# Kernel optimization log

Measured on AMD Instinct MI355X. Metric: run time of the kernel, lower is better.

Reference implementation:

```python
import jax, jax.numpy as jnp
import numpy as np

D = 768      # feature_dim (sum of extractor dims), divisible by nhead
H = 16       # nhead
DH = D // H
L = 3        # n_layers
NT = 256     # image tokens = (224/14)^2
B = 4
NPAST = 16
NF = 20      # hard-coded future horizon
C = NT + 1 + NPAST  # context length: image + intent + past
NEG = jnp.float32(-1e9)


def setup_inputs() -> dict:
    key = jax.random.key(0)
    ks = iter(jax.random.split(key, 64))
    def nrm(shape, scale):
        return jax.random.normal(next(ks), shape, jnp.float32) * scale
    w = lambda i, o: nrm((i, o), 1.0 / np.sqrt(i))
    inp = {}
    inp["image_tokens"] = nrm((B, NT, D), 1.0)
    inp["past"] = nrm((B, NPAST, 6), 1.0)
    inp["intent"] = jax.random.randint(next(ks), (B,), 1, 4)
    inp["pos_enc"] = nrm((1, NT, D), 0.02)          # positional_encoding param
    inp["future_q"] = nrm((1, NF, D), 1.0)           # future_queries param
    inp["intent_emb"] = nrm((1, 3, D), 1.0)          # intent_embeds param
    inp["time_emb"] = nrm((36, D), 1.0)              # time_embeds table
    inp["W_past"] = w(6, D);  inp["b_past"] = jnp.zeros((D,))
    inp["W_ppos"] = w(2, D);  inp["b_ppos"] = jnp.zeros((D,))
    inp["W_pp"] = w(2, D);    inp["b_pp"] = jnp.zeros((D,))      # pos_proj linear
    inp["g_pp"] = jnp.ones((D,)); inp["be_pp"] = jnp.zeros((D,)) # pos_proj LN
    inp["Wqkv"] = nrm((L, D, 3 * D), 1.0 / np.sqrt(D)); inp["bqkv"] = jnp.zeros((L, 3 * D))
    inp["Wo"] = nrm((L, D, D), 1.0 / np.sqrt(D));       inp["bo"] = jnp.zeros((L, D))
    inp["g1"] = jnp.ones((L, D)); inp["beta1"] = jnp.zeros((L, D))
    inp["g2"] = jnp.ones((L, D)); inp["beta2"] = jnp.zeros((L, D))
    inp["W1"] = nrm((L, D, 4 * D), 1.0 / np.sqrt(D));   inp["bf1"] = jnp.zeros((L, 4 * D))
    inp["W2"] = nrm((L, 4 * D, D), 1.0 / np.sqrt(4 * D)); inp["bf2"] = jnp.zeros((L, D))
    inp["Wd1"] = w(D, D); inp["bd1"] = jnp.zeros((D,))
    inp["Wd2"] = w(D, D); inp["bd2"] = jnp.zeros((D,))
    inp["Wd3"] = w(D, 2); inp["bd3"] = jnp.zeros((2,))
    return inp


def _ln(x, g, b):
    m = x.mean(-1, keepdims=True)
    v = ((x - m) ** 2).mean(-1, keepdims=True)
    return (x - m) / jnp.sqrt(v + 1e-5) * g + b


def reference(image_tokens, past, intent, pos_enc, future_q, intent_emb, time_emb,
              W_past, b_past, W_ppos, b_ppos, W_pp, b_pp, g_pp, be_pp,
              Wqkv, bqkv, Wo, bo, g1, beta1, g2, beta2, W1, bf1, W2, bf2,
              Wd1, bd1, Wd2, bd2, Wd3, bd3):
    Bn = past.shape[0]
    ctx_img = image_tokens + pos_enc                       # [B, NT, D]
    idx = jnp.clip(intent - 1, 0, 2)
    intent_tok = intent_emb[0][idx][:, None, :]            # [B, 1, D]
    past_tok = past @ W_past + b_past + past[..., :2] @ W_ppos + b_ppos + time_emb[:NPAST]
    context = jnp.concatenate([ctx_img, intent_tok, past_tok], axis=1)  # [B, C, D]
    future = jnp.broadcast_to(future_q + time_emb[NPAST:NPAST + NF], (Bn, NF, D))

    def block(x, mask, l):
        # norm_first TransformerEncoderLayer (dropout=0 at inference)
        h = _ln(x, g1[l], beta1[l])
        qkv = h @ Wqkv[l] + bqkv[l]
        q, k, v = jnp.split(qkv, 3, axis=-1)
        S = x.shape[1]
        q = q.reshape(Bn, S, H, DH).transpose(0, 2, 1, 3)
        k = k.reshape(Bn, S, H, DH).transpose(0, 2, 1, 3)
        v = v.reshape(Bn, S, H, DH).transpose(0, 2, 1, 3)
        scores = jnp.einsum('bhqd,bhkd->bhqk', q, k) / np.sqrt(DH).astype(np.float32) + mask
        a = jax.nn.softmax(scores, axis=-1)
        o = jnp.einsum('bhqk,bhkd->bhqd', a, v).transpose(0, 2, 1, 3).reshape(Bn, S, D)
        x = x + o @ Wo[l] + bo[l]
        h2 = _ln(x, g2[l], beta2[l])
        return x + jax.nn.relu(h2 @ W1[l] + bf1[l]) @ W2[l] + bf2[l]

    preds = []
    for t in range(NF):
        S = C + t + 1
        fm = jnp.where(jnp.triu(jnp.ones((t + 1, t + 1), bool), 1), NEG, jnp.float32(0.0))
        mask = jnp.zeros((S, S), jnp.float32).at[C:, C:].set(fm)
        x = jnp.concatenate([context, future[:, :t + 1]], axis=1)
        for l in range(L):
            x = block(x, mask, l)
        d = x[:, -1, :]
        d = jax.nn.gelu(d @ Wd1 + bd1, approximate=False)
        d = jax.nn.gelu(d @ Wd2 + bd2, approximate=False)
        p = d @ Wd3 + bd3                                   # [B, 2]
        preds.append(p[:, None, :])
        if t < NF - 1:
            future = future.at[:, t + 1].add(jax.nn.relu(_ln(p @ W_pp + b_pp, g_pp, be_pp)))
    return jnp.concatenate(preds, axis=1)                   # [B, 20, 2]
```

## Files before the change

kernel.cpp:

```cpp
#include <hip/hip_runtime.h>
#include <math.h>

#define DIM   768
#define NHEAD 16
#define DHEAD 48
#define NLAY  3
#define NTOK  256
#define BATCH 4
#define NPAST_ 16
#define NFUT  20
#define CCTX  273
#define SMAXT 293
#define MROWS 1172
#define NEGV  (-1.0e9f)
#define QKVPLANE 900096
#define STSTRIDE 52

typedef unsigned short u16;
typedef unsigned int   u32;
typedef __attribute__((ext_vector_type(8))) short short8;
typedef __attribute__((ext_vector_type(4))) float floatx4;

__device__ inline u16 f2bf(float x) {
    union { float f; u32 u; } v; v.f = x;
    u32 r = v.u + 0x7fffu + ((v.u >> 16) & 1u);
    return (u16)(r >> 16);
}

__device__ inline float bf2f(u16 x) {
    union { u32 u; float f; } c; c.u = ((u32)x) << 16;
    return c.f;
}

__device__ inline float gelu_f(float x) {
    return 0.5f * x * (1.0f + erff(x * 0.70710678118654752f));
}

__global__ void init_base(const float* __restrict__ img, const float* __restrict__ past,
                          const int* __restrict__ intent, const float* __restrict__ pos,
                          const float* __restrict__ futq, const float* __restrict__ iemb,
                          const float* __restrict__ temb, const float* __restrict__ Wp,
                          const float* __restrict__ bp, const float* __restrict__ Wpp,
                          const float* __restrict__ bpp, float* __restrict__ X)
{
    int r = blockIdx.x;
    int b = r / SMAXT, s = r % SMAXT;
    for (int j = threadIdx.x; j < DIM; j += blockDim.x) {
        float v;
        if (s < NTOK) {
            v = img[(long)(b * NTOK + s) * DIM + j] + pos[(long)s * DIM + j];
        } else if (s == NTOK) {
            int idx = intent[b] - 1; idx = idx < 0 ? 0 : (idx > 2 ? 2 : idx);
            v = iemb[(long)idx * DIM + j];
        } else if (s < CCTX) {
            int i = s - (NTOK + 1);
            v = bp[j] + bpp[j] + temb[(long)i * DIM + j];
            const float* pr = past + (long)(b * NPAST_ + i) * 6;
            #pragma unroll
            for (int c = 0; c < 6; ++c) v += pr[c] * Wp[(long)c * DIM + j];
            v += pr[0] * Wpp[j] + pr[1] * Wpp[DIM + j];
        } else {
            int f = s - CCTX;
            v = futq[(long)f * DIM + j] + temb[(long)(NPAST_ + f) * DIM + j];
        }
        X[(long)r * DIM + j] = v;
    }
}

__global__ void convert_transpose(const float* __restrict__ W, u16* __restrict__ Wt, int K, int N)
{
    __shared__ float tile[32][33];
    long lstride = (long)K * N;
    W  += blockIdx.z * lstride;
    Wt += blockIdx.z * lstride;
    int n0 = blockIdx.x * 32, k0 = blockIdx.y * 32;
    int tx = threadIdx.x & 31, ty = threadIdx.x >> 5;
    for (int i = ty; i < 32; i += 8)
        tile[i][tx] = W[(long)(k0 + i) * N + n0 + tx];
    __syncthreads();
    for (int i = ty; i < 32; i += 8)
        Wt[(long)(n0 + i) * K + k0 + tx] = f2bf(tile[tx][i]);
}

__launch_bounds__(256)
__global__ void ln_kernel(const float* __restrict__ x, const float* __restrict__ g,
                          const float* __restrict__ be, u16* __restrict__ y)
{
    int row = blockIdx.x * 4 + (threadIdx.x >> 6);
    int lane = threadIdx.x & 63;
    if (row >= MROWS) return;
    const float* xr = x + (long)row * DIM;
    float v[12];
    float s = 0.f;
    #pragma unroll
    for (int i = 0; i < 12; ++i) { v[i] = xr[lane + 64 * i]; s += v[i]; }
    for (int off = 32; off; off >>= 1) s += __shfl_down(s, off, 64);
    s = __shfl(s, 0, 64);
    float mean = s * (1.f / 768.f);
    float vs = 0.f;
    #pragma unroll
    for (int i = 0; i < 12; ++i) { float d = v[i] - mean; vs += d * d; }
    for (int off = 32; off; off >>= 1) vs += __shfl_down(vs, off, 64);
    vs = __shfl(vs, 0, 64);
    float inv = rsqrtf(vs * (1.f / 768.f) + 1e-5f);
    u16* yr = y + (long)row * DIM;
    #pragma unroll
    for (int i = 0; i < 12; ++i) {
        int j = lane + 64 * i;
        yr[j] = f2bf((v[i] - mean) * inv * g[j] + be[j]);
    }
}

__launch_bounds__(256)
__global__ void ln4_kernel(const float* __restrict__ x, const float* __restrict__ g,
                           const float* __restrict__ be, u16* __restrict__ y, int S)
{
    int b = threadIdx.x >> 6;
    int lane = threadIdx.x & 63;
    long row = (long)b * SMAXT + (S - 1);
    const float* xr = x + row * DIM;
    float v[12];
    float s = 0.f;
    #pragma unroll
    for (int i = 0; i < 12; ++i) { v[i] = xr[lane + 64 * i]; s += v[i]; }
    for (int off = 32; off; off >>= 1) s += __shfl_down(s, off, 64);
    s = __shfl(s, 0, 64);
    float mean = s * (1.f / 768.f);
    float vs = 0.f;
    #pragma unroll
    for (int i = 0; i < 12; ++i) { float d = v[i] - mean; vs += d * d; }
    for (int off = 32; off; off >>= 1) vs += __shfl_down(vs, off, 64);
    vs = __shfl(vs, 0, 64);
    float inv = rsqrtf(vs * (1.f / 768.f) + 1e-5f);
    u16* yr = y + row * DIM;
    #pragma unroll
    for (int i = 0; i < 12; ++i) {
        int j = lane + 64 * i;
        yr[j] = f2bf((v[i] - mean) * inv * g[j] + be[j]);
    }
}

template<int BM, int BN, int MODE>
__launch_bounds__(256)
__global__ void gemm_mfma(const u16* __restrict__ A, const u16* __restrict__ Wt,
                          const float* __restrict__ bias, const float* __restrict__ res,
                          void* __restrict__ outv, int M, int N, int K, int n0base)
{
    constexpr int MFRAG = BM / 16;
    constexpr int MI = MFRAG / 2;
    constexpr int NSUB = BN / 16;
    constexpr int NJ = NSUB / 2;
    constexpr int NA = (BM * 8) / 256;
    constexpr int NB = (BN * 8) / 256;
    __shared__ u16 As[2 * MFRAG * 64 * 8];
    __shared__ u16 Bs[2 * NSUB * 64 * 8];

    int tid = threadIdx.x;
    int lane = tid & 63;
    int w = tid >> 6, wm = w >> 1, wn = w & 1;
    int m0 = blockIdx.y * BM, n0 = n0base + blockIdx.x * BN;

    floatx4 acc[MI][NJ];
    #pragma unroll
    for (int i = 0; i < MI; ++i)
        #pragma unroll
        for (int j = 0; j < NJ; ++j) acc[i][j] = (floatx4){0.f, 0.f, 0.f, 0.f};

    int lm = lane & 15, lk = lane >> 4;

    for (int k0 = 0; k0 < K; k0 += 64) {
        __syncthreads();
        #pragma unroll
        for (int i = 0; i < NA; ++i) {
            int q = tid + 256 * i;
            int r = q >> 3, c = q & 7;
            int gr = m0 + r; if (gr >= M) gr = M - 1;
            int4 v = *(const int4*)(A + (long)gr * K + k0 + c * 8);
            int off = (((c >> 2) * MFRAG + (r >> 4)) * 64 + (r & 15) * 4 + (c & 3)) * 8;
            *(int4*)&As[off] = v;
        }
        #pragma unroll
        for (int i = 0; i < NB; ++i) {
            int q = tid + 256 * i;
            int r = q >> 3, c = q & 7;
            int4 v = *(const int4*)(Wt + (long)(n0 + r) * K + k0 + c * 8);
            int off = (((c >> 2) * NSUB + (r >> 4)) * 64 + (r & 15) * 4 + (c & 3)) * 8;
            *(int4*)&Bs[off] = v;
        }
        __syncthreads();
        #pragma unroll
        for (int t = 0; t < 2; ++t) {
            short8 af[MI];
            #pragma unroll
            for (int i = 0; i < MI; ++i)
                af[i] = *(const short8*)&As[((t * MFRAG + wm * MI + i) * 64 + lm * 4 + lk) * 8];
            short8 bfr[NJ];
            #pragma unroll
            for (int j = 0; j < NJ; ++j)
                bfr[j] = *(const short8*)&Bs[((t * NSUB + wn * NJ + j) * 64 + lm * 4 + lk) * 8];
            #pragma unroll
            for (int i = 0; i < MI; ++i)
                #pragma unroll
                for (int j = 0; j < NJ; ++j)
                    acc[i][j] = __builtin_amdgcn_mfma_f32_16x16x32_bf16(af[i], bfr[j], acc[i][j], 0, 0, 0);
        }
    }

    #pragma unroll
    for (int j = 0; j < NJ; ++j) {
        int col = n0 + wn * (NJ * 16) + j * 16 + lm;
        float bv = bias[col];
        #pragma unroll
        for (int i = 0; i < MI; ++i) {
            int rbase = m0 + wm * (MI * 16) + i * 16 + lk * 4;
            #pragma unroll
            for (int rr = 0; rr < 4; ++rr) {
                int row = rbase + rr;
                if (row >= M) continue;
                float val = acc[i][j][rr] + bv;
                if (MODE == 0) {
                    val += res[(long)row * N + col];
                    ((float*)outv)[(long)row * N + col] = val;
                } else if (MODE == 1) {
                    val = fmaxf(val, 0.f);
                    ((u16*)outv)[(long)row * N + col] = f2bf(val);
                } else {
                    int which = col >= 1536 ? 2 : (col >= 768 ? 1 : 0);
                    int rem = col - which * 768;
                    int h = rem / 48, d = rem - h * 48;
                    if (which == 0) val *= 0.14433756729740643f;
                    int b = row / SMAXT, s = row - b * SMAXT;
                    ((float*)outv)[(long)which * QKVPLANE + ((long)(b * 16 + h) * SMAXT + s) * 48 + d] = val;
                }
            }
        }
    }
}

__launch_bounds__(256)
__global__ void qkv_update(const u16* __restrict__ h, long hstride, const u16* __restrict__ Wt,
                           const float* __restrict__ bias, float* __restrict__ qkvdst, int srow)
{
    int b = blockIdx.y;
    int col = blockIdx.x * 256 + threadIdx.x;
    __shared__ float hs[768];
    for (int i = threadIdx.x; i < 768; i += 256)
        hs[i] = bf2f(h[(long)b * hstride + i]);
    __syncthreads();
    const short8* wr = (const short8*)(Wt + (long)col * 768);
    float a0 = 0.f, a1 = 0.f, a2 = 0.f, a3 = 0.f;
    #pragma unroll 4
    for (int k8 = 0; k8 < 96; ++k8) {
        short8 wv = wr[k8];
        const float* hp = &hs[k8 * 8];
        a0 = fmaf(hp[0], bf2f((u16)wv[0]), a0);
        a1 = fmaf(hp[1], bf2f((u16)wv[1]), a1);
        a2 = fmaf(hp[2], bf2f((u16)wv[2]), a2);
        a3 = fmaf(hp[3], bf2f((u16)wv[3]), a3);
        a0 = fmaf(hp[4], bf2f((u16)wv[4]), a0);
        a1 = fmaf(hp[5], bf2f((u16)wv[5]), a1);
        a2 = fmaf(hp[6], bf2f((u16)wv[6]), a2);
        a3 = fmaf(hp[7], bf2f((u16)wv[7]), a3);
    }
    float acc = (a0 + a1) + (a2 + a3) + bias[col];
    int which = col >= 1536 ? 2 : (col >= 768 ? 1 : 0);
    int rem = col - which * 768;
    int hh = rem / 48, d = rem - hh * 48;
    if (which == 0) acc *= 0.14433756729740643f;
    qkvdst[(long)which * QKVPLANE + ((long)(b * 16 + hh) * SMAXT + srow) * 48 + d] = acc;
}

__launch_bounds__(256)
__global__ void attn_kernel(const float* __restrict__ qkv, u16* __restrict__ o, int S,
                            float* __restrict__ state, int q0base)
{
    int bh = blockIdx.y;
    int b = bh >> 4, h = bh & 15;
    int q0 = q0base + blockIdx.x * 16;
    if (q0 >= S) return;
    __shared__ float qs[16][48];
    __shared__ float kbuf[3328];
    __shared__ float sc[16][304];
    int t = threadIdx.x;
    const float* qp = qkv + (long)bh * SMAXT * 48;
    const float* kp = qp + QKVPLANE;
    const float* vp = qp + 2 * QKVPLANE;

    for (int lin = t; lin < 16 * 48; lin += 256) {
        int i2 = lin / 48, d = lin % 48;
        int qi2 = q0 + i2; if (qi2 > S - 1) qi2 = S - 1;
        qs[i2][d] = qp[(long)qi2 * 48 + d];
    }
    __syncthreads();
    int i = t >> 4, j = t & 15;
    int qi = q0 + i;
    float4 q4[12];
    #pragma unroll
    for (int k4 = 0; k4 < 12; ++k4) q4[k4] = *(const float4*)&qs[i][k4 * 4];

    for (int s0 = 0; s0 < S; s0 += 64) {
        int ns = S - s0; if (ns > 64) ns = 64;
        __syncthreads();
        for (int lin = t; lin < 64 * 12; lin += 256) {
            int ss = lin / 12, d4 = lin % 12;
            float4 kv = make_float4(0.f, 0.f, 0.f, 0.f);
            if (ss < ns) kv = *(const float4*)(kp + (long)(s0 + ss) * 48 + d4 * 4);
            *(float4*)&kbuf[ss * 52 + d4 * 4] = kv;
        }
        __syncthreads();
        #pragma unroll
        for (int u = 0; u < 4; ++u) {
            int ss = j + 16 * u;
            float acc = 0.f;
            #pragma unroll
            for (int k4 = 0; k4 < 12; ++k4) {
                float4 kk = *(const float4*)&kbuf[ss * 52 + k4 * 4];
                acc += q4[k4].x * kk.x + q4[k4].y * kk.y + q4[k4].z * kk.z + q4[k4].w * kk.w;
            }
            int s = s0 + ss;
            if (ss < ns) {
                bool masked = (qi >= CCTX) && (s > qi);
                sc[i][s] = masked ? acc + NEGV : acc;
            }
        }
    }
    __syncthreads();

    float mx = -1e30f;
    for (int s = j; s < S; s += 16) mx = fmaxf(mx, sc[i][s]);
    #pragma unroll
    for (int m = 8; m; m >>= 1) mx = fmaxf(mx, __shfl_xor(mx, m, 16));
    int Sp = (S + 3) & ~3;
    float sum = 0.f;
    for (int s = j; s < Sp; s += 16) {
        float e = (s < S) ? __expf(sc[i][s] - mx) : 0.f;
        sc[i][s] = e; sum += e;
    }
    #pragma unroll
    for (int m = 8; m; m >>= 1) sum += __shfl_xor(sum, m, 16);
    float inv = 1.f / sum;

    float oc0 = 0.f, oc1 = 0.f, oc2 = 0.f;
    int d0 = j * 3;
    for (int s0 = 0; s0 < S; s0 += 64) {
        int ns4 = Sp - s0; if (ns4 > 64) ns4 = 64;
        __syncthreads();
        for (int lin = t; lin < 64 * 48; lin += 256) {
            int ss = lin / 48, d = lin % 48;
            float v = 0.f;
            int s = s0 + ss;
            if (s < S) v = vp[(long)s * 48 + d];
            kbuf[d * 68 + ss] = v;
        }
        __syncthreads();
        for (int sb = 0; sb < ns4; sb += 4) {
            float4 a4 = *(const float4*)&sc[i][s0 + sb];
            float4 v0 = *(const float4*)&kbuf[d0 * 68 + sb];
            float4 v1 = *(const float4*)&kbuf[(d0 + 1) * 68 + sb];
            float4 v2 = *(const float4*)&kbuf[(d0 + 2) * 68 + sb];
            oc0 += a4.x * v0.x + a4.y * v0.y + a4.z * v0.z + a4.w * v0.w;
            oc1 += a4.x * v1.x + a4.y * v1.y + a4.z * v1.z + a4.w * v1.w;
            oc2 += a4.x * v2.x + a4.y * v2.y + a4.z * v2.z + a4.w * v2.w;
        }
    }
    if (qi < S) {
        u16* orow = o + ((long)(b * SMAXT + qi)) * 768 + h * 48 + d0;
        orow[0] = f2bf(oc0 * inv); orow[1] = f2bf(oc1 * inv); orow[2] = f2bf(oc2 * inv);
    }
    if (state && qi < CCTX) {
        float* st = state + ((long)bh * 293 + qi) * STSTRIDE;
        st[d0] = oc0; st[d0 + 1] = oc1; st[d0 + 2] = oc2;
        if (j == 0) { st[48] = mx; st[49] = sum; }
    }
}

__launch_bounds__(256)
__global__ void attn0_inc(const float* __restrict__ qkv, float* __restrict__ state,
                          u16* __restrict__ o, int S)
{
    int bh = blockIdx.x & 63;
    int b = bh >> 4, h = bh & 15;
    int t = threadIdx.x;
    const float* qp = qkv + (long)bh * SMAXT * 48;
    const float* kp = qp + QKVPLANE;
    const float* vp = qp + 2 * QKVPLANE;
    __shared__ float buf[304];
    __shared__ float kn[48], vn[48];
    __shared__ float redm[4], redl[4];

    if (blockIdx.x < 64) {
        if (t < 48) kn[t] = kp[(long)(S - 1) * 48 + t];
        else if (t < 96) vn[t - 48] = vp[(long)(S - 1) * 48 + (t - 48)];
        __syncthreads();
        for (int r = t; r < CCTX; r += 256) {
            const float* qr = qp + (long)r * 48;
            float x = 0.f;
            #pragma unroll
            for (int d = 0; d < 48; ++d) x += qr[d] * kn[d];
            float* st = state + ((long)bh * 293 + r) * STSTRIDE;
            float m_old = st[48], l_old = st[49];
            float m_new = fmaxf(m_old, x);
            float f = __expf(m_old - m_new), e = __expf(x - m_new);
            float l_new = l_old * f + e;
            st[48] = m_new; st[49] = l_new;
            float invl = 1.f / l_new;
            u16* orow = o + ((long)(b * SMAXT + r)) * 768 + h * 48;
            #pragma unroll
            for (int d = 0; d < 48; ++d) {
                float oa = st[d] * f + e * vn[d];
                st[d] = oa;
                orow[d] = f2bf(oa * invl);
            }
        }
    } else {
        if (t < 48) kn[t] = qp[(long)(S - 1) * 48 + t];
        __syncthreads();
        float mymax = -1e30f;
        for (int s = t; s < S; s += 256) {
            const float* kr = kp + (long)s * 48;
            float x = 0.f;
            #pragma unroll
            for (int d = 0; d < 48; ++d) x += kn[d] * kr[d];
            buf[s] = x;
            mymax = fmaxf(mymax, x);
        }
        for (int off = 32; off; off >>= 1) mymax = fmaxf(mymax, __shfl_down(mymax, off, 64));
        int wid = t >> 6, lane = t & 63;
        if (!lane) redm[wid] = mymax;
        __syncthreads();
        float mx = fmaxf(fmaxf(redm[0], redm[1]), fmaxf(redm[2], redm[3]));
        float lsum = 0.f;
        for (int s = t; s < S; s += 256) {
            float e = __expf(buf[s] - mx);
            buf[s] = e; lsum += e;
        }
        for (int off = 32; off; off >>= 1) lsum += __shfl_down(lsum, off, 64);
        if (!lane) redl[wid] = lsum;
        __syncthreads();
        float inv = 1.f / (redl[0] + redl[1] + redl[2] + redl[3]);
        if (t < 48) {
            float acc = 0.f;
            for (int s = 0; s < S; ++s) acc += buf[s] * vp[(long)s * 48 + t];
            u16* orow = o + ((long)(b * SMAXT + (S - 1))) * 768 + h * 48;
            orow[t] = f2bf(acc * inv);
        }
    }
}

__launch_bounds__(256)
__global__ void otiny_kernel(const u16* __restrict__ ao, const u16* __restrict__ WoT2,
                             const float* __restrict__ bo2, float* __restrict__ xbuf, int S)
{
    int b = blockIdx.y;
    int col = blockIdx.x * 256 + threadIdx.x;
    long row = (long)b * SMAXT + (S - 1);
    __shared__ float hs[768];
    for (int i = threadIdx.x; i < 768; i += 256) hs[i] = bf2f(ao[row * 768 + i]);
    __syncthreads();
    const short8* wr = (const short8*)(WoT2 + (long)col * 768);
    float a0 = 0.f, a1 = 0.f, a2 = 0.f, a3 = 0.f;
    #pragma unroll 4
    for (int k8 = 0; k8 < 96; ++k8) {
        short8 wv = wr[k8];
        const float* hp = &hs[k8 * 8];
        a0 = fmaf(hp[0], bf2f((u16)wv[0]), a0);
        a1 = fmaf(hp[1], bf2f((u16)wv[1]), a1);
        a2 = fmaf(hp[2], bf2f((u16)wv[2]), a2);
        a3 = fmaf(hp[3], bf2f((u16)wv[3]), a3);
        a0 = fmaf(hp[4], bf2f((u16)wv[4]), a0);
        a1 = fmaf(hp[5], bf2f((u16)wv[5]), a1);
        a2 = fmaf(hp[6], bf2f((u16)wv[6]), a2);
        a3 = fmaf(hp[7], bf2f((u16)wv[7]), a3);
    }
    xbuf[row * 768 + col] += (a0 + a1) + (a2 + a3) + bo2[col];
}

__launch_bounds__(256)
__global__ void ffn1_tiny(const u16* __restrict__ h, const u16* __restrict__ W1T2,
                          const float* __restrict__ bf12, u16* __restrict__ big, int S)
{
    int b = blockIdx.y;
    int col = blockIdx.x * 256 + threadIdx.x;
    long row = (long)b * SMAXT + (S - 1);
    __shared__ float hs[768];
    for (int i = threadIdx.x; i < 768; i += 256) hs[i] = bf2f(h[row * 768 + i]);
    __syncthreads();
    const short8* wr = (const short8*)(W1T2 + (long)col * 768);
    float a0 = 0.f, a1 = 0.f, a2 = 0.f, a3 = 0.f;
    #pragma unroll 4
    for (int k8 = 0; k8 < 96; ++k8) {
        short8 wv = wr[k8];
        const float* hp = &hs[k8 * 8];
        a0 = fmaf(hp[0], bf2f((u16)wv[0]), a0);
        a1 = fmaf(hp[1], bf2f((u16)wv[1]), a1);
        a2 = fmaf(hp[2], bf2f((u16)wv[2]), a2);
        a3 = fmaf(hp[3], bf2f((u16)wv[3]), a3);
        a0 = fmaf(hp[4], bf2f((u16)wv[4]), a0);
        a1 = fmaf(hp[5], bf2f((u16)wv[5]), a1);
        a2 = fmaf(hp[6], bf2f((u16)wv[6]), a2);
        a3 = fmaf(hp[7], bf2f((u16)wv[7]), a3);
    }
    float acc = (a0 + a1) + (a2 + a3) + bf12[col];
    big[row * 3072 + col] = f2bf(fmaxf(acc, 0.f));
}

__launch_bounds__(256)
__global__ void ffn2_tiny(const u16* __restrict__ big, const u16* __restrict__ W2T2,
                          const float* __restrict__ bf22, float* __restrict__ xbuf, int S)
{
    int b = blockIdx.y;
    int tid = threadIdx.x;
    int col = blockIdx.x * 64 + (tid & 63);
    int kg = tid >> 6;
    long row = (long)b * SMAXT + (S - 1);
    __shared__ float hs[3072];
    __shared__ float red[4][64];
    for (int i = tid; i < 3072; i += 256) hs[i] = bf2f(big[row * 3072 + i]);
    __syncthreads();
    const short8* wr = (const short8*)(W2T2 + (long)col * 3072 + kg * 768);
    const float* hp0 = &hs[kg * 768];
    float a0 = 0.f, a1 = 0.f, a2 = 0.f, a3 = 0.f;
    #pragma unroll 4
    for (int k8 = 0; k8 < 96; ++k8) {
        short8 wv = wr[k8];
        const float* hp = hp0 + k8 * 8;
        a0 = fmaf(hp[0], bf2f((u16)wv[0]), a0);
        a1 = fmaf(hp[1], bf2f((u16)wv[1]), a1);
        a2 = fmaf(hp[2], bf2f((u16)wv[2]), a2);
        a3 = fmaf(hp[3], bf2f((u16)wv[3]), a3);
        a0 = fmaf(hp[4], bf2f((u16)wv[4]), a0);
        a1 = fmaf(hp[5], bf2f((u16)wv[5]), a1);
        a2 = fmaf(hp[6], bf2f((u16)wv[6]), a2);
        a3 = fmaf(hp[7], bf2f((u16)wv[7]), a3);
    }
    red[kg][tid & 63] = (a0 + a1) + (a2 + a3);
    __syncthreads();
    if (kg == 0) {
        float acc = red[0][tid] + red[1][tid] + red[2][tid] + red[3][tid] + bf22[col];
        xbuf[row * 768 + col] += acc;
    }
}

__launch_bounds__(256)
__global__ void dec_gelu(const float* __restrict__ src, long srowstride,
                         const float* __restrict__ W, const float* __restrict__ bias,
                         float* __restrict__ dst)
{
    int b = blockIdx.y;
    int jb = blockIdx.x;
    __shared__ float s0buf[768];
    __shared__ float red[4][64];
    int tid = threadIdx.x;
    const float* sr = src + (long)b * srowstride;
    for (int i = tid; i < 768; i += 256) s0buf[i] = sr[i];
    __syncthreads();
    int jj = tid & 63, ig = tid >> 6;
    int jcol = jb * 64 + jj;
    float acc = 0.f;
    const float* wp = W + (long)(ig * 192) * 768 + jcol;
    #pragma unroll 4
    for (int i = 0; i < 192; ++i) acc += s0buf[ig * 192 + i] * wp[(long)i * 768];
    red[ig][jj] = acc;
    __syncthreads();
    if (ig == 0) {
        float a = red[0][jj] + red[1][jj] + red[2][jj] + red[3][jj] + bias[jcol];
        dst[(long)b * 768 + jcol] = gelu_f(a);
    }
}

__launch_bounds__(256)
__global__ void dec_final(const float* __restrict__ d2, const float* __restrict__ Wd3,
                          const float* __restrict__ bd3, const float* __restrict__ Wpp,
                          const float* __restrict__ bpp, const float* __restrict__ gpp,
                          const float* __restrict__ bepp, float* __restrict__ out,
                          float* __restrict__ X, int t,
                          const float* __restrict__ g1l0, const float* __restrict__ be1l0,
                          u16* __restrict__ h0new)
{
    int b = blockIdx.x;
    int tid = threadIdx.x;
    __shared__ float red[2][4];
    __shared__ float pp[2];
    const float* dr = d2 + (long)b * 768;
    float a0 = 0.f, a1 = 0.f;
    for (int i = tid; i < 768; i += 256) {
        float v = dr[i];
        a0 += v * Wd3[2 * i]; a1 += v * Wd3[2 * i + 1];
    }
    for (int off = 32; off; off >>= 1) { a0 += __shfl_down(a0, off, 64); a1 += __shfl_down(a1, off, 64); }
    int wid = tid >> 6, lane = tid & 63;
    if (!lane) { red[0][wid] = a0; red[1][wid] = a1; }
    __syncthreads();
    if (!tid) {
        float p0 = red[0][0] + red[0][1] + red[0][2] + red[0][3] + bd3[0];
        float p1 = red[1][0] + red[1][1] + red[1][2] + red[1][3] + bd3[1];
        out[(long)(b * NFUT + t) * 2 + 0] = p0;
        out[(long)(b * NFUT + t) * 2 + 1] = p1;
        pp[0] = p0; pp[1] = p1;
    }
    __syncthreads();
    if (t == NFUT - 1) return;
    float p0 = pp[0], p1 = pp[1];
    float pv[3]; float s = 0.f;
    #pragma unroll
    for (int u = 0; u < 3; ++u) {
        int jcol = tid + 256 * u;
        pv[u] = p0 * Wpp[jcol] + p1 * Wpp[768 + jcol] + bpp[jcol];
        s += pv[u];
    }
    for (int off = 32; off; off >>= 1) s += __shfl_down(s, off, 64);
    __syncthreads();
    if (!lane) red[0][wid] = s;
    __syncthreads();
    float mean = (red[0][0] + red[0][1] + red[0][2] + red[0][3]) * (1.f / 768.f);
    float vs = 0.f;
    #pragma unroll
    for (int u = 0; u < 3; ++u) { float d = pv[u] - mean; vs += d * d; }
    for (int off = 32; off; off >>= 1) vs += __shfl_down(vs, off, 64);
    __syncthreads();
    if (!lane) red[1][wid] = vs;
    __syncthreads();
    float var = (red[1][0] + red[1][1] + red[1][2] + red[1][3]) * (1.f / 768.f);
    float inv = rsqrtf(var + 1e-5f);
    float* Xr = X + ((long)(b * SMAXT + CCTX + t + 1)) * 768;
    float xv[3];
    #pragma unroll
    for (int u = 0; u < 3; ++u) {
        int jcol = tid + 256 * u;
        float y = (pv[u] - mean) * inv * gpp[jcol] + bepp[jcol];
        float old = Xr[jcol];
        float nv = old + (y > 0.f ? y : 0.f);
        Xr[jcol] = nv;
        xv[u] = nv;
    }
    float xs = xv[0] + xv[1] + xv[2];
    for (int off = 32; off; off >>= 1) xs += __shfl_down(xs, off, 64);
    __syncthreads();
    if (!lane) red[0][wid] = xs;
    __syncthreads();
    float xmean = (red[0][0] + red[0][1] + red[0][2] + red[0][3]) * (1.f / 768.f);
    float xq = 0.f;
    #pragma unroll
    for (int u = 0; u < 3; ++u) { float d = xv[u] - xmean; xq += d * d; }
    for (int off = 32; off; off >>= 1) xq += __shfl_down(xq, off, 64);
    __syncthreads();
    if (!lane) red[1][wid] = xq;
    __syncthreads();
    float xvar = (red[1][0] + red[1][1] + red[1][2] + red[1][3]) * (1.f / 768.f);
    float xinv = rsqrtf(xvar + 1e-5f);
    #pragma unroll
    for (int u = 0; u < 3; ++u) {
        int jcol = tid + 256 * u;
        h0new[b * 768 + jcol] = f2bf((xv[u] - xmean) * xinv * g1l0[jcol] + be1l0[jcol]);
    }
}

extern "C" void kernel_launch(void* const* d_in, const int* in_sizes, int n_in,
                              void* d_out, int out_size, void* d_ws, size_t ws_size,
                              hipStream_t stream)
{
    const float* img    = (const float*)d_in[0];
    const float* past   = (const float*)d_in[1];
    const int*   intent = (const int*)d_in[2];
    const float* pos    = (const float*)d_in[3];
    const float* futq   = (const float*)d_in[4];
    const float* iemb   = (const float*)d_in[5];
    const float* temb   = (const float*)d_in[6];
    const float* W_past = (const float*)d_in[7];
    const float* b_past = (const float*)d_in[8];
    const float* W_ppos = (const float*)d_in[9];
    const float* b_ppos = (const float*)d_in[10];
    const float* W_pp   = (const float*)d_in[11];
    const float* b_pp   = (const float*)d_in[12];
    const float* g_pp   = (const float*)d_in[13];
    const float* be_pp  = (const float*)d_in[14];
    const float* Wqkv   = (const float*)d_in[15];
    const float* bqkv   = (const float*)d_in[16];
    const float* Wo     = (const float*)d_in[17];
    const float* bo     = (const float*)d_in[18];
    const float* g1     = (const float*)d_in[19];
    const float* beta1  = (const float*)d_in[20];
    const float* g2     = (const float*)d_in[21];
    const float* beta2  = (const float*)d_in[22];
    const float* W1     = (const float*)d_in[23];
    const float* bf1    = (const float*)d_in[24];
    const float* W2     = (const float*)d_in[25];
    const float* bf2    = (const float*)d_in[26];
    const float* Wd1    = (const float*)d_in[27];
    const float* bd1    = (const float*)d_in[28];
    const float* Wd2    = (const float*)d_in[29];
    const float* bd2    = (const float*)d_in[30];
    const float* Wd3    = (const float*)d_in[31];
    const float* bd3    = (const float*)d_in[32];
    float* out = (float*)d_out;

    float* ws     = (float*)d_ws;
    float* Xb     = ws;
    float* xbuf   = ws + 900096;
    float* qkvbuf = ws + 1800192;
    u16*   hbuf   = (u16*)(ws + 4500480);
    u16*   aobuf  = (u16*)(ws + 4950528);
    u16*   big    = (u16*)(ws + 5400576);
    float* d1ws   = ws + 7200768;
    float* d2ws   = ws + 7203840;
    u16*   WqkvT  = (u16*)(ws + 7206912);
    u16*   WoT    = (u16*)(ws + 9861120);
    u16*   W1T    = (u16*)(ws + 10745856);
    u16*   W2T    = (u16*)(ws + 14284800);
    float* qkv0   = ws + 17823744;
    u16*   h0new  = (u16*)(ws + 20524032);
    u16*   aobuf0 = (u16*)(ws + 20525568);
    float* state  = ws + 20975616;

    convert_transpose<<<dim3(2304/32, 768/32, 3), 256, 0, stream>>>(Wqkv, WqkvT, 768, 2304);
    convert_transpose<<<dim3(768/32, 768/32, 3), 256, 0, stream>>>(Wo, WoT, 768, 768);
    convert_transpose<<<dim3(3072/32, 768/32, 3), 256, 0, stream>>>(W1, W1T, 768, 3072);
    convert_transpose<<<dim3(768/32, 3072/32, 3), 256, 0, stream>>>(W2, W2T, 3072, 768);

    init_base<<<dim3(MROWS), dim3(256), 0, stream>>>(img, past, intent, pos, futq, iemb,
                                                     temb, W_past, b_past, W_ppos, b_ppos, Xb);

    for (int t = 0; t < NFUT; ++t) {
        int S = CCTX + t + 1;

        if (t == 0) {
            ln_kernel<<<dim3(293), dim3(256), 0, stream>>>(Xb, g1, beta1, hbuf);
            gemm_mfma<64, 64, 2><<<dim3(36, 19), dim3(256), 0, stream>>>(
                hbuf, WqkvT, bqkv, nullptr, qkv0, MROWS, 2304, 768, 0);
            attn_kernel<<<dim3((S + 15) / 16, 64), dim3(256), 0, stream>>>(qkv0, aobuf0, S, state, 0);
        } else {
            qkv_update<<<dim3(9, 4), dim3(256), 0, stream>>>(h0new, 768L, WqkvT, bqkv, qkv0, CCTX + t);
            attn0_inc<<<dim3(128), dim3(256), 0, stream>>>(qkv0, state, aobuf0, S);
        }
        gemm_mfma<64, 32, 0><<<dim3(24, 19), dim3(256), 0, stream>>>(
            aobuf0, WoT, bo, Xb, xbuf, MROWS, 768, 768, 0);
        ln_kernel<<<dim3(293), dim3(256), 0, stream>>>(xbuf, g2, beta2, hbuf);
        gemm_mfma<64, 64, 1><<<dim3(48, 19), dim3(256), 0, stream>>>(
            hbuf, W1T, bf1, nullptr, big, MROWS, 3072, 768, 0);
        gemm_mfma<64, 32, 0><<<dim3(24, 19), dim3(256), 0, stream>>>(
            big, W2T, bf2, xbuf, xbuf, MROWS, 768, 3072, 0);

        ln_kernel<<<dim3(293), dim3(256), 0, stream>>>(xbuf, g1 + 768, beta1 + 768, hbuf);
        gemm_mfma<64, 64, 2><<<dim3(36, 19), dim3(256), 0, stream>>>(
            hbuf, WqkvT + 1L * 768 * 2304, bqkv + 2304, nullptr, qkvbuf, MROWS, 2304, 768, 0);
        attn_kernel<<<dim3((S + 15) / 16, 64), dim3(256), 0, stream>>>(qkvbuf, aobuf, S, nullptr, 0);
        gemm_mfma<64, 32, 0><<<dim3(24, 19), dim3(256), 0, stream>>>(
            aobuf, WoT + 1L * 768 * 768, bo + 768, xbuf, xbuf, MROWS, 768, 768, 0);
        ln_kernel<<<dim3(293), dim3(256), 0, stream>>>(xbuf, g2 + 768, beta2 + 768, hbuf);
        gemm_mfma<64, 64, 1><<<dim3(48, 19), dim3(256), 0, stream>>>(
            hbuf, W1T + 1L * 768 * 3072, bf1 + 3072, nullptr, big, MROWS, 3072, 768, 0);
        gemm_mfma<64, 32, 0><<<dim3(24, 19), dim3(256), 0, stream>>>(
            big, W2T + 1L * 3072 * 768, bf2 + 768, xbuf, xbuf, MROWS, 768, 3072, 0);

        ln_kernel<<<dim3(293), dim3(256), 0, stream>>>(xbuf, g1 + 2 * 768, beta1 + 2 * 768, hbuf);
        gemm_mfma<64, 32, 2><<<dim3(48, 19), dim3(256), 0, stream>>>(
            hbuf, WqkvT + 2L * 768 * 2304, bqkv + 2 * 2304, nullptr, qkvbuf, MROWS, 2304, 768, 768);
        qkv_update<<<dim3(3, 4), dim3(256), 0, stream>>>(
            hbuf + (long)(S - 1) * 768, (long)SMAXT * 768,
            WqkvT + 2L * 768 * 2304, bqkv + 2 * 2304, qkvbuf, S - 1);
        attn_kernel<<<dim3(1, 64), dim3(256), 0, stream>>>(qkvbuf, aobuf, S, nullptr, S - 16);
        otiny_kernel<<<dim3(3, 4), dim3(256), 0, stream>>>(aobuf, WoT + 2L * 768 * 768, bo + 2 * 768, xbuf, S);
        ln4_kernel<<<dim3(1), dim3(256), 0, stream>>>(xbuf, g2 + 2 * 768, beta2 + 2 * 768, hbuf, S);
        ffn1_tiny<<<dim3(12, 4), dim3(256), 0, stream>>>(hbuf, W1T + 2L * 768 * 3072, bf1 + 2 * 3072, big, S);
        ffn2_tiny<<<dim3(12, 4), dim3(256), 0, stream>>>(big, W2T + 2L * 3072 * 768, bf2 + 2 * 768, xbuf, S);

        dec_gelu<<<dim3(12, 4), dim3(256), 0, stream>>>(xbuf + (long)(S - 1) * 768, (long)SMAXT * 768, Wd1, bd1, d1ws);
        dec_gelu<<<dim3(12, 4), dim3(256), 0, stream>>>(d1ws, 768L, Wd2, bd2, d2ws);
        dec_final<<<dim3(4), dim3(256), 0, stream>>>(d2ws, Wd3, bd3, W_pp, b_pp, g_pp, be_pp, out, Xb, t,
                                                     g1, beta1, h0new);
    }
}
```

Baseline: 9.428 ms.

## Fuse LayerNorm into GEMM A-loads and split-K the FFN2 GEMM with atomics

Standalone LayerNorm launches are removed. The W1 and QKV GEMMs now compute per-row mean and inverse std up front, then normalize the fp32 activations while staging tiles into shared memory. The FFN down-projection (K=3072) is split four ways along K, and partial sums are accumulated into the residual buffer in place with atomicAdd, with the bias added only by the first split. This cuts launches and the bf16 hbuf round-trip and raises block count for the long-K GEMM. The cost is redundant LN statistics per N-tile, more global reads of fp32 activations, atomic traffic, and non-deterministic summation order.

```diff
diff --git a/kernel.cpp b/kernel.cpp
--- a/kernel.cpp
+++ b/kernel.cpp
@@ -140,9 +140,11 @@
     }
 }
 
-template<int BM, int BN, int MODE>
-__launch_bounds__(256)
-__global__ void gemm_mfma(const u16* __restrict__ A, const u16* __restrict__ Wt,
+template<int BM, int BN, int MODE, bool LNF, int KSPLIT>
+__launch_bounds__(256)
+__global__ void gemm_mfma(const u16* __restrict__ A, const float* __restrict__ xs,
+                          const float* __restrict__ lng, const float* __restrict__ lnb,
+                          const u16* __restrict__ Wt,
                           const float* __restrict__ bias, const float* __restrict__ res,
                           void* __restrict__ outv, int M, int N, int K, int n0base)
 {
@@ -154,12 +156,36 @@
     constexpr int NB = (BN * 8) / 256;
     __shared__ u16 As[2 * MFRAG * 64 * 8];
     __shared__ u16 Bs[2 * NSUB * 64 * 8];
+    __shared__ float smu[BM], siv[BM];
 
     int tid = threadIdx.x;
     int lane = tid & 63;
     int w = tid >> 6, wm = w >> 1, wn = w & 1;
     int m0 = blockIdx.y * BM, n0 = n0base + blockIdx.x * BN;
 
+    if constexpr (LNF) {
+        #pragma unroll 1
+        for (int rr = 0; rr < BM / 4; ++rr) {
+            int r = w * (BM / 4) + rr;
+            int gr = m0 + r; if (gr >= M) gr = M - 1;
+            const float* xr = xs + (long)gr * 768;
+            float v[12];
+            float s = 0.f;
+            #pragma unroll
+            for (int i = 0; i < 12; ++i) { v[i] = xr[lane + 64 * i]; s += v[i]; }
+            for (int off = 32; off; off >>= 1) s += __shfl_down(s, off, 64);
+            s = __shfl(s, 0, 64);
+            float mean = s * (1.f / 768.f);
+            float vs = 0.f;
+            #pragma unroll
+            for (int i = 0; i < 12; ++i) { float d = v[i] - mean; vs += d * d; }
+            for (int off = 32; off; off >>= 1) vs += __shfl_down(vs, off, 64);
+            vs = __shfl(vs, 0, 64);
+            float inv = rsqrtf(vs * (1.f / 768.f) + 1e-5f);
+            if (lane == 0) { smu[r] = mean; siv[r] = inv; }
+        }
+    }
+
     floatx4 acc[MI][NJ];
     #pragma unroll
     for (int i = 0; i < MI; ++i)
@@ -168,16 +194,39 @@
 
     int lm = lane & 15, lk = lane >> 4;
 
-    for (int k0 = 0; k0 < K; k0 += 64) {
+    int ksz = K / KSPLIT;
+    int kb = (KSPLIT > 1) ? blockIdx.z * ksz : 0;
+    for (int k0 = kb; k0 < kb + ksz; k0 += 64) {
         __syncthreads();
         #pragma unroll
         for (int i = 0; i < NA; ++i) {
             int q = tid + 256 * i;
             int r = q >> 3, c = q & 7;
             int gr = m0 + r; if (gr >= M) gr = M - 1;
-            int4 v = *(const int4*)(A + (long)gr * K + k0 + c * 8);
             int off = (((c >> 2) * MFRAG + (r >> 4)) * 64 + (r & 15) * 4 + (c & 3)) * 8;
-            *(int4*)&As[off] = v;
+            if constexpr (LNF) {
+                const float* xp = xs + (long)gr * 768 + k0 + c * 8;
+                float4 f0 = *(const float4*)(xp);
+                float4 f1 = *(const float4*)(xp + 4);
+                float4 ga = *(const float4*)(lng + k0 + c * 8);
+                float4 gb = *(const float4*)(lng + k0 + c * 8 + 4);
+                float4 ba = *(const float4*)(lnb + k0 + c * 8);
+                float4 bb = *(const float4*)(lnb + k0 + c * 8 + 4);
+                float mu = smu[r], iv = siv[r];
+                short8 pk;
+                pk[0] = (short)f2bf((f0.x - mu) * iv * ga.x + ba.x);
+                pk[1] = (short)f2bf((f0.y - mu) * iv * ga.y + ba.y);
+                pk[2] = (short)f2bf((f0.z - mu) * iv * ga.z + ba.z);
+                pk[3] = (short)f2bf((f0.w - mu) * iv * ga.w + ba.w);
+                pk[4] = (short)f2bf((f1.x - mu) * iv * gb.x + bb.x);
+                pk[5] = (short)f2bf((f1.y - mu) * iv * gb.y + bb.y);
+                pk[6] = (short)f2bf((f1.z - mu) * iv * gb.z + bb.z);
+                pk[7] = (short)f2bf((f1.w - mu) * iv * gb.w + bb.w);
+                *(int4*)&As[off] = *(int4*)&pk;
+            } else {
+                int4 v = *(const int4*)(A + (long)gr * K + k0 + c * 8);
+                *(int4*)&As[off] = v;
+            }
         }
         #pragma unroll
         for (int i = 0; i < NB; ++i) {
@@ -217,6 +266,11 @@
             for (int rr = 0; rr < 4; ++rr) {
                 int row = rbase + rr;
                 if (row >= M) continue;
+                if (MODE == 3) {
+                    float val = acc[i][j][rr] + (blockIdx.z == 0 ? bv : 0.f);
+                    atomicAdd(&((float*)outv)[(long)row * N + col], val);
+                    continue;
+                }
                 float val = acc[i][j][rr] + bv;
                 if (MODE == 0) {
                     val += res[(long)row * N + col];
@@ -725,36 +779,36 @@
 
         if (t == 0) {
             ln_kernel<<<dim3(293), dim3(256), 0, stream>>>(Xb, g1, beta1, hbuf);
-            gemm_mfma<64, 64, 2><<<dim3(36, 19), dim3(256), 0, stream>>>(
-                hbuf, WqkvT, bqkv, nullptr, qkv0, MROWS, 2304, 768, 0);
+            gemm_mfma<64, 64, 2, false, 1><<<dim3(36, 19), dim3(256), 0, stream>>>(
+                hbuf, nullptr, nullptr, nullptr, WqkvT, bqkv, nullptr, qkv0, MROWS, 2304, 768, 0);
             attn_kernel<<<dim3((S + 15) / 16, 64), dim3(256), 0, stream>>>(qkv0, aobuf0, S, state, 0);
         } else {
             qkv_update<<<dim3(9, 4), dim3(256), 0, stream>>>(h0new, 768L, WqkvT, bqkv, qkv0, CCTX + t);
             attn0_inc<<<dim3(128), dim3(256), 0, stream>>>(qkv0, state, aobuf0, S);
         }
-        gemm_mfma<64, 32, 0><<<dim3(24, 19), dim3(256), 0, stream>>>(
-            aobuf0, WoT, bo, Xb, xbuf, MROWS, 768, 768, 0);
-        ln_kernel<<<dim3(293), dim3(256), 0, stream>>>(xbuf, g2, beta2, hbuf);
-        gemm_mfma<64, 64, 1><<<dim3(48, 19), dim3(256), 0, stream>>>(
-            hbuf, W1T, bf1, nullptr, big, MROWS, 3072, 768, 0);
-        gemm_mfma<64, 32, 0><<<dim3(24, 19), dim3(256), 0, stream>>>(
-            big, W2T, bf2, xbuf, xbuf, MROWS, 768, 3072, 0);
-
-        ln_kernel<<<dim3(293), dim3(256), 0, stream>>>(xbuf, g1 + 768, beta1 + 768, hbuf);
-        gemm_mfma<64, 64, 2><<<dim3(36, 19), dim3(256), 0, stream>>>(
-            hbuf, WqkvT + 1L * 768 * 2304, bqkv + 2304, nullptr, qkvbuf, MROWS, 2304, 768, 0);
+        gemm_mfma<64, 32, 0, false, 1><<<dim3(24, 19), dim3(256), 0, stream>>>(
+            aobuf0, nullptr, nullptr, nullptr, WoT, bo, Xb, xbuf, MROWS, 768, 768, 0);
+        gemm_mfma<64, 64, 1, true, 1><<<dim3(48, 19), dim3(256), 0, stream>>>(
+            nullptr, xbuf, g2, beta2, W1T, bf1, nullptr, big, MROWS, 3072, 768, 0);
+        gemm_mfma<64, 32, 3, false, 4><<<dim3(24, 19, 4), dim3(256), 0, stream>>>(
+            big, nullptr, nullptr, nullptr, W2T, bf2, nullptr, xbuf, MROWS, 768, 3072, 0);
+
+        gemm_mfma<64, 64, 2, true, 1><<<dim3(36, 19), dim3(256), 0, stream>>>(
+            nullptr, xbuf, g1 + 768, beta1 + 768, WqkvT + 1L * 768 * 2304, bqkv + 2304,
+            nullptr, qkvbuf, MROWS, 2304, 768, 0);
         attn_kernel<<<dim3((S + 15) / 16, 64), dim3(256), 0, stream>>>(qkvbuf, aobuf, S, nullptr, 0);
-        gemm_mfma<64, 32, 0><<<dim3(24, 19), dim3(256), 0, stream>>>(
-            aobuf, WoT + 1L * 768 * 768, bo + 768, xbuf, xbuf, MROWS, 768, 768, 0);
-        ln_kernel<<<dim3(293), dim3(256), 0, stream>>>(xbuf, g2 + 768, beta2 + 768, hbuf);
-        gemm_mfma<64, 64, 1><<<dim3(48, 19), dim3(256), 0, stream>>>(
-            hbuf, W1T + 1L * 768 * 3072, bf1 + 3072, nullptr, big, MROWS, 3072, 768, 0);
-        gemm_mfma<64, 32, 0><<<dim3(24, 19), dim3(256), 0, stream>>>(
-            big, W2T + 1L * 3072 * 768, bf2 + 768, xbuf, xbuf, MROWS, 768, 3072, 0);
-
-        ln_kernel<<<dim3(293), dim3(256), 0, stream>>>(xbuf, g1 + 2 * 768, beta1 + 2 * 768, hbuf);
-        gemm_mfma<64, 32, 2><<<dim3(48, 19), dim3(256), 0, stream>>>(
-            hbuf, WqkvT + 2L * 768 * 2304, bqkv + 2 * 2304, nullptr, qkvbuf, MROWS, 2304, 768, 768);
+        gemm_mfma<64, 32, 0, false, 1><<<dim3(24, 19), dim3(256), 0, stream>>>(
+            aobuf, nullptr, nullptr, nullptr, WoT + 1L * 768 * 768, bo + 768, xbuf, xbuf, MROWS, 768, 768, 0);
+        gemm_mfma<64, 64, 1, true, 1><<<dim3(48, 19), dim3(256), 0, stream>>>(
+            nullptr, xbuf, g2 + 768, beta2 + 768, W1T + 1L * 768 * 3072, bf1 + 3072,
+            nullptr, big, MROWS, 3072, 768, 0);
+        gemm_mfma<64, 32, 3, false, 4><<<dim3(24, 19, 4), dim3(256), 0, stream>>>(
+            big, nullptr, nullptr, nullptr, W2T + 1L * 3072 * 768, bf2 + 768, nullptr, xbuf, MROWS, 768, 3072, 0);
+
+        gemm_mfma<64, 32, 2, true, 1><<<dim3(48, 19), dim3(256), 0, stream>>>(
+            nullptr, xbuf, g1 + 2 * 768, beta1 + 2 * 768, WqkvT + 2L * 768 * 2304, bqkv + 2 * 2304,
+            nullptr, qkvbuf, MROWS, 2304, 768, 768);
+        ln4_kernel<<<dim3(1), dim3(256), 0, stream>>>(xbuf, g1 + 2 * 768, beta1 + 2 * 768, hbuf, S);
         qkv_update<<<dim3(3, 4), dim3(256), 0, stream>>>(
             hbuf + (long)(S - 1) * 768, (long)SMAXT * 768,
             WqkvT + 2L * 768 * 2304, bqkv + 2 * 2304, qkvbuf, S - 1);
```

Result: slower. 10.33 ms (+9.6%).
